# Kernel tuning notes

Hardware: AMD Instinct MI355X
Metric: run time of the kernel (lower is better)

## Reference

```python
import jax, jax.numpy as jnp
import numpy as np
import math

H = 12          # num_heads
HD = 64         # head_dim
M = 32          # random features = head_dim * kernel_ratio
EPS = 1e-8


def prm_exp(x, w):
    # x: [B,H,T,HD], w: [H,M,HD] -> [B,H,T,M]
    xd = 0.5 * jnp.sum(x * x, axis=-1, keepdims=True)        # [B,H,T,1]
    wtx = jnp.einsum('bhti,hmi->bhtm', x, w)                  # [B,H,T,M]
    return jnp.exp(wtx - xd) / math.sqrt(M)


def setup_inputs() -> dict:
    key = jax.random.key(0)
    ks = jax.random.split(key, 5)
    B, N, C = 8, 4096, 768
    x = jax.random.normal(ks[0], (B, N, C), dtype=jnp.float32)
    kqv_w = jax.random.normal(ks[1], (3 * C, C), dtype=jnp.float32) * (1.0 / math.sqrt(C))
    kqv_b = jnp.zeros((3 * C,), dtype=jnp.float32)
    proj_w = jax.random.normal(ks[2], (C, C), dtype=jnp.float32) * (1.0 / math.sqrt(C))
    proj_b = jnp.zeros((C,), dtype=jnp.float32)
    # frozen random-feature matrix: orthogonal rows per head, scaled by sqrt(M)
    wr = jax.random.normal(ks[3], (H, M, HD), dtype=jnp.float32)
    q_ortho, _ = jnp.linalg.qr(jnp.swapaxes(wr, -1, -2))       # [H,HD,M], cols orthonormal
    w = jnp.swapaxes(q_ortho, -1, -2) * math.sqrt(M)           # [H,M,HD]
    return {"x": x, "kqv_w": kqv_w, "kqv_b": kqv_b,
            "proj_w": proj_w, "proj_b": proj_b, "w": w}


def reference(x, kqv_w, kqv_b, proj_w, proj_b, w):
    B, N, C = x.shape
    kqv = x @ kqv_w.T + kqv_b                                  # [B,N,3C]
    kqv = kqv.reshape(B, N, 3, H, HD).transpose(2, 0, 3, 1, 4) # [3,B,H,N,HD]
    k, q, v = kqv[0], kqv[1], kqv[2]
    kp = prm_exp(k, w)                                         # [B,H,N,M]
    qp = prm_exp(q, w)                                         # [B,H,N,M]
    D = jnp.einsum('bhtm,bhm->bht', qp, kp.sum(axis=2))[..., None]   # [B,H,N,1]
    kptv = jnp.einsum('bhin,bhim->bhnm', v, kp)                # [B,H,HD,M]
    y = jnp.einsum('bhtm,bhnm->bhtn', qp, kptv) / (D + EPS)    # [B,H,N,HD]
    y = y.transpose(0, 2, 1, 3).reshape(B, N, C)
    y = y @ proj_w.T + proj_b
    return y
```

## Files before the change

kernel.cpp:

```cpp
#include <hip/hip_runtime.h>
#include <math.h>

namespace {
constexpr int cB  = 8;
constexpr int cN  = 4096;
constexpr int cC  = 768;
constexpr int cH  = 12;
constexpr int cHD = 64;
constexpr int cM  = 32;
}

typedef __attribute__((ext_vector_type(8))) short bf16x8;
typedef __attribute__((ext_vector_type(4))) float f32x4;

#define BARRIER() do { asm volatile("" ::: "memory"); __builtin_amdgcn_s_barrier(); asm volatile("" ::: "memory"); } while (0)
#define WAIT_VM(N) do { asm volatile("s_waitcnt vmcnt(" #N ")" ::: "memory"); __builtin_amdgcn_sched_barrier(0); } while (0)
#define WAIT_LGKM0() do { asm volatile("s_waitcnt lgkmcnt(0)" ::: "memory"); __builtin_amdgcn_sched_barrier(0); } while (0)

__device__ __forceinline__ void async_copy16(const void* g, void* l) {
    __builtin_amdgcn_global_load_lds((const __attribute__((address_space(1))) void*)g,
                                     (__attribute__((address_space(3))) void*)l, 16, 0, 0);
}

__device__ __forceinline__ ushort f32_to_bf16_rne(float x) {
    unsigned int u = __float_as_uint(x);
    u += 0x7fffu + ((u >> 16) & 1u);
    return (ushort)(u >> 16);
}

__device__ __forceinline__ float bf16_to_f32(ushort u) {
    return __uint_as_float(((unsigned)u) << 16);
}

__device__ __forceinline__ void split2(float f, ushort& h, ushort& l) {
    h = f32_to_bf16_rne(f);
    float r = f - bf16_to_f32(h);
    l = f32_to_bf16_rne(r);
}

__global__ __launch_bounds__(256)
void split_bf16(const float* __restrict__ in, ushort* __restrict__ hi,
                ushort* __restrict__ lo, int n4)
{
    int i = blockIdx.x * 256 + threadIdx.x;
    const int stride = gridDim.x * 256;
    for (; i < n4; i += stride) {
        float4 v = reinterpret_cast<const float4*>(in)[i];
        ushort4 h, l;
        split2(v.x, h.x, l.x);
        split2(v.y, h.y, l.y);
        split2(v.z, h.z, l.z);
        split2(v.w, h.w, l.w);
        reinterpret_cast<ushort4*>(hi)[i] = h;
        reinterpret_cast<ushort4*>(lo)[i] = l;
    }
}

template <int TERMS, int FUSE>
__global__ __launch_bounds__(512, 2)
void gemm256(const ushort* __restrict__ Ah, const ushort* __restrict__ Al,
             const ushort* __restrict__ Bh, const ushort* __restrict__ Bl,
             const float* __restrict__ bias,
             float* __restrict__ Cf, ushort* __restrict__ Cb,
             int Ndim, int K, int mode,
             ushort* __restrict__ kp, ushort* __restrict__ qp,
             float* __restrict__ kpsum_p,
             const ushort* __restrict__ whb, const ushort* __restrict__ wlb)
{
    constexpr int APL = (TERMS >= 2) ? 2 : 1;
    constexpr int BPL = (TERMS == 3) ? 2 : 1;
    constexpr int NPL = APL + BPL;
    __shared__ ushort smem[2 * NPL * 8192];
    const int tid = threadIdx.x;
    const int wave = tid >> 6, lane = tid & 63;
    const int wm = wave >> 2, wn = wave & 3;
    const int fr = lane & 15, fk = lane >> 4;
    const int fco = (fk ^ ((fr >> 1) & 3)) * 8;

    const int nwg = gridDim.x * 128;
    const int orig = blockIdx.x * 128 + blockIdx.y;
    const int swz = (orig & 7) * (nwg >> 3) + (orig >> 3);
    const int row0 = (swz & 127) << 8;
    const int col0 = (swz >> 7) << 8;

    const ushort* planes[NPL];
    if constexpr (TERMS == 3) { planes[0] = Ah; planes[1] = Al; planes[2] = Bh; planes[3] = Bl; }
    else { planes[0] = Ah; planes[1] = Bh; }

    const ushort* gsrc[NPL][2];
    int ldst[NPL][2];
    #pragma unroll
    for (int p = 0; p < NPL; ++p)
        #pragma unroll
        for (int h2 = 0; h2 < 2; ++h2) {
            const int ci = h2 * 512 + tid;
            const int row = ci >> 2;
            const int cc = (ci & 3) ^ ((row >> 1) & 3);
            const int grow = ((p < APL) ? row0 : col0) + row;
            gsrc[p][h2] = planes[p] + (size_t)grow * K + cc * 8;
            ldst[p][h2] = p * 8192 + h2 * 4096 + wave * 512;
        }

    const int NT = K >> 5;
    f32x4 acc[8][4] = {};

    #pragma unroll
    for (int p = 0; p < NPL; ++p)
        #pragma unroll
        for (int h2 = 0; h2 < 2; ++h2)
            async_copy16(gsrc[p][h2], &smem[ldst[p][h2]]);
    #pragma unroll
    for (int p = 0; p < NPL; ++p)
        #pragma unroll
        for (int h2 = 0; h2 < 2; ++h2)
            async_copy16(gsrc[p][h2] + 32, &smem[NPL * 8192 + ldst[p][h2]]);
    if constexpr (TERMS == 3) WAIT_VM(8); else WAIT_VM(4);
    BARRIER();

    for (int t = 0; t < NT; ++t) {
        const int cb = (t & 1) * NPL * 8192;
        const int nb = ((t + 1) & 1) * NPL * 8192;
        bf16x8 fb[4][BPL];
        #pragma unroll
        for (int mp = 0; mp < 4; ++mp) {
            if (mp == 0) {
                #pragma unroll
                for (int ni = 0; ni < 4; ++ni) {
                    const int off = cb + APL * 8192 + (wn * 64 + ni * 16 + fr) * 32 + fco;
                    fb[ni][0] = *reinterpret_cast<const bf16x8*>(&smem[off]);
                    if constexpr (BPL == 2)
                        fb[ni][1] = *reinterpret_cast<const bf16x8*>(&smem[off + 8192]);
                }
            }
            bf16x8 fa[2][APL];
            #pragma unroll
            for (int m2 = 0; m2 < 2; ++m2) {
                const int off = cb + (wm * 128 + (mp * 2 + m2) * 16 + fr) * 32 + fco;
                fa[m2][0] = *reinterpret_cast<const bf16x8*>(&smem[off]);
                if constexpr (APL == 2)
                    fa[m2][1] = *reinterpret_cast<const bf16x8*>(&smem[off + 8192]);
            }
            if (t >= 1 && t + 1 < NT && mp < APL) {
                async_copy16(gsrc[mp][0] + (t + 1) * 32, &smem[nb + ldst[mp][0]]);
                async_copy16(gsrc[mp][1] + (t + 1) * 32, &smem[nb + ldst[mp][1]]);
            }
            if (t + 2 < NT && mp >= APL && mp < APL + BPL) {
                async_copy16(gsrc[mp][0] + (t + 2) * 32, &smem[cb + ldst[mp][0]]);
                async_copy16(gsrc[mp][1] + (t + 2) * 32, &smem[cb + ldst[mp][1]]);
            }
            BARRIER();
            WAIT_LGKM0();
            __builtin_amdgcn_s_setprio(1);
            #pragma unroll
            for (int term = 0; term < TERMS; ++term) {
                const int pa = (TERMS == 3) ? ((term == 2) ? 1 : 0) : 0;
                const int pb = (TERMS == 3) ? ((term == 1) ? 1 : 0) : 0;
                #pragma unroll
                for (int m2 = 0; m2 < 2; ++m2)
                    #pragma unroll
                    for (int ni = 0; ni < 4; ++ni)
                        acc[mp * 2 + m2][ni] = __builtin_amdgcn_mfma_f32_16x16x32_bf16(
                            fa[m2][pa], fb[ni][pb], acc[mp * 2 + m2][ni], 0, 0, 0);
            }
            __builtin_amdgcn_s_setprio(0);
            if (mp == 3) {
                if (t + 2 < NT)      { if constexpr (BPL == 2) WAIT_VM(4); else WAIT_VM(2); }
                else if (t + 1 < NT) { WAIT_VM(0); }
            }
            if (mp < 3 || t + 1 < NT) BARRIER();
        }
    }

    if constexpr (FUSE) {
        BARRIER();
        const int cglob = col0 + wn * 64;
        const bool is_k = (cglob < 768);
        const int h = (is_k ? cglob : cglob - 768) >> 6;
        const int rbase = row0 + wm * 128;
        const int b = rbase >> 12;
        const int bh = b * cH + h;
        const int trow0 = rbase & 4095;
        ushort* phi = is_k ? kp : qp;
        bf16x8 Wh2[2][2], Wl2[2][2];
        #pragma unroll
        for (int mf = 0; mf < 2; ++mf)
            #pragma unroll
            for (int kc = 0; kc < 2; ++kc) {
                size_t off = (size_t)(h * 32 + mf * 16 + fr) * 64 + kc * 32 + fk * 8;
                Wh2[mf][kc] = *reinterpret_cast<const bf16x8*>(&whb[off]);
                Wl2[mf][kc] = *reinterpret_cast<const bf16x8*>(&wlb[off]);
            }
        unsigned* kt = reinterpret_cast<unsigned*>(&smem[wave * 8192]);
        const float rsm = 0.17677669529663687f;
        #pragma unroll
        for (int pass = 0; pass < 2; ++pass) {
            #pragma unroll
            for (int ni = 0; ni < 4; ++ni) {
                const float bv = bias[cglob + ni * 16 + fr];
                #pragma unroll
                for (int mi = 0; mi < 4; ++mi) {
                    #pragma unroll
                    for (int j = 0; j < 4; ++j) {
                        const int rrow = mi * 16 + fk * 4 + j;
                        const int ccol = ni * 16 + fr;
                        ushort hh, ll;
                        split2(acc[pass * 4 + mi][ni][j] + bv, hh, ll);
                        const int ccs = (ccol >> 2) ^ (rrow & 15);
                        kt[rrow * 64 + ccs * 4 + (ccol & 3)] = ((unsigned)ll << 16) | hh;
                    }
                }
            }
            f32x4 acc2[4][2] = {};
            float xdv4[4];
            #pragma unroll
            for (int tf = 0; tf < 4; ++tf) {
                const int rrow = tf * 16 + fr;
                const unsigned* rowp = &kt[rrow * 64];
                uint4 c0 = *reinterpret_cast<const uint4*>(&rowp[(((fk << 1))     ^ fr) << 2]);
                uint4 c1 = *reinterpret_cast<const uint4*>(&rowp[(((fk << 1) | 1) ^ fr) << 2]);
                uint4 c2 = *reinterpret_cast<const uint4*>(&rowp[(((fk << 1) + 8) ^ fr) << 2]);
                uint4 c3 = *reinterpret_cast<const uint4*>(&rowp[(((fk << 1) + 9) ^ fr) << 2]);
                unsigned u[16] = {c0.x,c0.y,c0.z,c0.w, c1.x,c1.y,c1.z,c1.w,
                                  c2.x,c2.y,c2.z,c2.w, c3.x,c3.y,c3.z,c3.w};
                bf16x8 Ah2[2], Al2[2];
                float xs = 0.f;
                #pragma unroll
                for (int e = 0; e < 16; ++e) {
                    const ushort hh = (ushort)(u[e] & 0xffffu);
                    const ushort ll = (ushort)(u[e] >> 16);
                    Ah2[e >> 3][e & 7] = (short)hh;
                    Al2[e >> 3][e & 7] = (short)ll;
                    const float kv = bf16_to_f32(hh) + bf16_to_f32(ll);
                    xs = fmaf(kv, kv, xs);
                }
                xs += __shfl_xor(xs, 16);
                xs += __shfl_xor(xs, 32);
                xdv4[tf] = 0.5f * xs;
                #pragma unroll
                for (int kc = 0; kc < 2; ++kc)
                    #pragma unroll
                    for (int mf = 0; mf < 2; ++mf) {
                        acc2[tf][mf] = __builtin_amdgcn_mfma_f32_16x16x32_bf16(Ah2[kc], Wh2[mf][kc], acc2[tf][mf], 0, 0, 0);
                        acc2[tf][mf] = __builtin_amdgcn_mfma_f32_16x16x32_bf16(Ah2[kc], Wl2[mf][kc], acc2[tf][mf], 0, 0, 0);
                        acc2[tf][mf] = __builtin_amdgcn_mfma_f32_16x16x32_bf16(Al2[kc], Wh2[mf][kc], acc2[tf][mf], 0, 0, 0);
                    }
            }
            float sm0 = 0.f, sm1 = 0.f;
            #pragma unroll
            for (int tf = 0; tf < 4; ++tf) {
                #pragma unroll
                for (int j = 0; j < 4; ++j) {
                    const int rloc = fk * 4 + j;
                    const float xdv = __shfl(xdv4[tf], (lane & 48) | rloc);
                    const int tg = trow0 + pass * 64 + tf * 16 + rloc;
                    float e0 = __expf(acc2[tf][0][j] - xdv) * rsm;
                    float e1 = __expf(acc2[tf][1][j] - xdv) * rsm;
                    phi[((size_t)bh * cN + tg) * cM + fr]      = f32_to_bf16_rne(e0);
                    phi[((size_t)bh * cN + tg) * cM + 16 + fr] = f32_to_bf16_rne(e1);
                    sm0 += e0; sm1 += e1;
                }
            }
            if (is_k) {
                sm0 += __shfl_xor(sm0, 16); sm0 += __shfl_xor(sm0, 32);
                sm1 += __shfl_xor(sm1, 16); sm1 += __shfl_xor(sm1, 32);
                const int tblk = (trow0 + pass * 64) >> 6;
                if (lane < 16) {
                    kpsum_p[((size_t)bh * 64 + tblk) * cM + lane]      = sm0;
                    kpsum_p[((size_t)bh * 64 + tblk) * cM + 16 + lane] = sm1;
                }
            }
        }
        return;
    }

    #pragma unroll
    for (int ni = 0; ni < 4; ++ni) {
        const int c = col0 + wn * 64 + ni * 16 + fr;
        const float bv = bias[c];
        #pragma unroll
        for (int mi = 0; mi < 8; ++mi) {
            const int r0 = row0 + wm * 128 + mi * 16 + fk * 4;
            #pragma unroll
            for (int j = 0; j < 4; ++j) {
                const float val = acc[mi][ni][j] + bv;
                const int row = r0 + j;
                if (mode == 0) {
                    Cf[(size_t)row * Ndim + c] = val;
                } else {
                    const int b = row >> 12, tt = row & 4095;
                    const int h = c >> 6, d = c & 63;
                    Cb[(((size_t)(b * cH + h) * cN + tt) << 6) + d] = f32_to_bf16_rne(val);
                }
            }
        }
    }
}

__global__ __launch_bounds__(64)
void pv_mfma(const ushort* __restrict__ qp, const ushort* __restrict__ kptvx,
             ushort* __restrict__ yh)
{
    const int bh = blockIdx.x, tblk = blockIdx.y;
    const int b = bh / cH, h = bh % cH;
    const int t0 = tblk * 64;
    const int lane = threadIdx.x;
    const int fr = lane & 15, fk = lane >> 4;
    bf16x8 Bf[5];
    #pragma unroll
    for (int nf = 0; nf < 5; ++nf)
        Bf[nf] = *reinterpret_cast<const bf16x8*>(&kptvx[(size_t)bh * 2560 + (nf * 16 + fr) * 32 + fk * 8]);
    f32x4 acc[4][5] = {};
    #pragma unroll
    for (int tf = 0; tf < 4; ++tf) {
        bf16x8 Af = *reinterpret_cast<const bf16x8*>(&qp[((size_t)bh * cN + t0 + tf * 16 + fr) * cM + fk * 8]);
        #pragma unroll
        for (int nf = 0; nf < 5; ++nf)
            acc[tf][nf] = __builtin_amdgcn_mfma_f32_16x16x32_bf16(Af, Bf[nf], acc[tf][nf], 0, 0, 0);
    }
    #pragma unroll
    for (int tf = 0; tf < 4; ++tf) {
        #pragma unroll
        for (int j = 0; j < 4; ++j) {
            const int rloc = (lane >> 4) * 4 + j;
            const int t = t0 + tf * 16 + rloc;
            const float Dv = __shfl(acc[tf][4][j], lane & 48) + 1e-8f;
            const float rD = 1.0f / Dv;
            #pragma unroll
            for (int nf = 0; nf < 4; ++nf) {
                float yv = acc[tf][nf][j] * rD;
                size_t oa = (size_t)(b * cN + t) * cC + h * 64 + nf * 16 + fr;
                yh[oa] = f32_to_bf16_rne(yv);
            }
        }
    }
}

__global__ __launch_bounds__(256, 4)
void kptv_part(const ushort* __restrict__ vbf, const ushort* __restrict__ kp,
               float* __restrict__ kptv_p)
{
    const int bh = blockIdx.x, chunk = blockIdx.y;
    __shared__ float vl[64][68];
    __shared__ float kl[64][36];
    const int tid = threadIdx.x;
    const int half = tid >> 7;
    const int dg = (tid >> 3) & 15;
    const int mg = tid & 7;
    float acc[4][4] = {};
    for (int tile = 0; tile < 8; ++tile) {
        const int tb = chunk * 512 + tile * 64;
        #pragma unroll
        for (int i = 0; i < 2; ++i) {
            int idx = i * 256 + tid;
            int row = idx >> 3, seg = idx & 7;
            bf16x8 vv = *reinterpret_cast<const bf16x8*>(&vbf[((size_t)bh * cN + tb + row) * 64 + seg * 8]);
            float4 lo4 = make_float4(bf16_to_f32((ushort)vv[0]), bf16_to_f32((ushort)vv[1]),
                                     bf16_to_f32((ushort)vv[2]), bf16_to_f32((ushort)vv[3]));
            float4 hi4 = make_float4(bf16_to_f32((ushort)vv[4]), bf16_to_f32((ushort)vv[5]),
                                     bf16_to_f32((ushort)vv[6]), bf16_to_f32((ushort)vv[7]));
            *reinterpret_cast<float4*>(&vl[row][seg * 8])     = lo4;
            *reinterpret_cast<float4*>(&vl[row][seg * 8 + 4]) = hi4;
        }
        {
            int row = tid >> 2, seg = tid & 3;
            bf16x8 vv = *reinterpret_cast<const bf16x8*>(&kp[((size_t)bh * cN + tb + row) * 32 + seg * 8]);
            float4 lo4 = make_float4(bf16_to_f32((ushort)vv[0]), bf16_to_f32((ushort)vv[1]),
                                     bf16_to_f32((ushort)vv[2]), bf16_to_f32((ushort)vv[3]));
            float4 hi4 = make_float4(bf16_to_f32((ushort)vv[4]), bf16_to_f32((ushort)vv[5]),
                                     bf16_to_f32((ushort)vv[6]), bf16_to_f32((ushort)vv[7]));
            *reinterpret_cast<float4*>(&kl[row][seg * 8])     = lo4;
            *reinterpret_cast<float4*>(&kl[row][seg * 8 + 4]) = hi4;
        }
        __syncthreads();
        for (int t = 0; t < 32; ++t) {
            const int tt = half * 32 + t;
            float4 av = *reinterpret_cast<const float4*>(&vl[tt][dg * 4]);
            float4 bv = *reinterpret_cast<const float4*>(&kl[tt][mg * 4]);
            float a4[4] = {av.x, av.y, av.z, av.w};
            float b4[4] = {bv.x, bv.y, bv.z, bv.w};
            #pragma unroll
            for (int i = 0; i < 4; ++i)
                #pragma unroll
                for (int j = 0; j < 4; ++j)
                    acc[i][j] = fmaf(a4[i], b4[j], acc[i][j]);
        }
        __syncthreads();
    }
    float* outp = &kptv_p[(((size_t)chunk * 2 + half) * 96 + bh) * 2048];
    #pragma unroll
    for (int i = 0; i < 4; ++i)
        *reinterpret_cast<float4*>(&outp[(dg * 4 + i) * 32 + mg * 4]) =
            make_float4(acc[i][0], acc[i][1], acc[i][2], acc[i][3]);
}

__global__ __launch_bounds__(256)
void kptv_reduce(const float* __restrict__ kptv_p, const float* __restrict__ kpsum_p,
                 ushort* __restrict__ kptvx)
{
    const int bh = blockIdx.x, tid = threadIdx.x;
    for (int l = tid; l < 2048; l += 256) {
        float s = 0.f;
        #pragma unroll
        for (int c = 0; c < 16; ++c) s += kptv_p[((size_t)c * 96 + bh) * 2048 + l];
        kptvx[(size_t)bh * 2560 + l] = f32_to_bf16_rne(s);
    }
    if (tid < 32) {
        float s = 0.f;
        #pragma unroll
        for (int c = 0; c < 64; ++c) s += kpsum_p[((size_t)bh * 64 + c) * cM + tid];
        kptvx[(size_t)bh * 2560 + 64 * 32 + tid] = f32_to_bf16_rne(s);
    }
    for (int l = tid; l < 480; l += 256)
        kptvx[(size_t)bh * 2560 + 65 * 32 + l] = 0;
}

extern "C" void kernel_launch(void* const* d_in, const int* in_sizes, int n_in,
                              void* d_out, int out_size, void* d_ws, size_t ws_size,
                              hipStream_t stream)
{
    const float* x      = (const float*)d_in[0];
    const float* kqv_w  = (const float*)d_in[1];
    const float* kqv_b  = (const float*)d_in[2];
    const float* proj_w = (const float*)d_in[3];
    const float* proj_b = (const float*)d_in[4];
    const float* w      = (const float*)d_in[5];

    char* wsb = (char*)d_ws;
    ushort* xh   = (ushort*)(wsb);
    ushort* xl   = (ushort*)(wsb + 50331648);
    ushort* yh   = (ushort*)(wsb + 100663296);
    ushort* vbf  = (ushort*)(wsb + 201326592);
    ushort* wh   = (ushort*)(wsb + 251658240);
    ushort* wl_  = (ushort*)(wsb + 255197184);
    ushort* pwh  = (ushort*)(wsb + 258736128);
    ushort* pwl  = (ushort*)(wsb + 259915776);
    ushort* whb  = (ushort*)(wsb + 261095424);
    ushort* wlb  = (ushort*)(wsb + 261144576);

    char* ob = (char*)d_out;
    ushort* kp      = (ushort*)ob;
    ushort* qp      = (ushort*)(ob + 25165824);
    float*  kptv_p  = (float*)(ob + 50331648);
    float*  kpsum_p = (float*)(ob + 62914560);
    ushort* kptvx   = (ushort*)(ob + 63700992);
    float*  out     = (float*)d_out;

    dim3 blk(256);
    split_bf16<<<2048, blk, 0, stream>>>(x, xh, xl, 25165824 / 4);
    split_bf16<<<1728, blk, 0, stream>>>(kqv_w, wh, wl_, 1769472 / 4);
    split_bf16<<<576, blk, 0, stream>>>(proj_w, pwh, pwl, 589824 / 4);
    split_bf16<<<24, blk, 0, stream>>>(w, whb, wlb, 24576 / 4);
    gemm256<3, 1><<<dim3(6, 128), dim3(512), 0, stream>>>(
        xh, xl, wh, wl_, kqv_b, nullptr, nullptr, 1536, 768, 0,
        kp, qp, kpsum_p, whb, wlb);
    gemm256<1, 0><<<dim3(3, 128), dim3(512), 0, stream>>>(
        xh, nullptr, wh + (size_t)1536 * 768, nullptr, kqv_b + 1536,
        nullptr, vbf, 768, 768, 2, nullptr, nullptr, nullptr, nullptr, nullptr);
    kptv_part<<<dim3(96, 8), blk, 0, stream>>>(vbf, kp, kptv_p);
    kptv_reduce<<<dim3(96), blk, 0, stream>>>(kptv_p, kpsum_p, kptvx);
    pv_mfma<<<dim3(96, 64), dim3(64), 0, stream>>>(qp, kptvx, yh);
    gemm256<1, 0><<<dim3(3, 128), dim3(512), 0, stream>>>(
        yh, nullptr, pwh, nullptr, proj_b, out, nullptr, 768, 768, 0,
        nullptr, nullptr, nullptr, nullptr, nullptr);
}
```

Before: 438.8 us.

## Compute K^T V with MFMA on transposed kp/v layouts

The fused GEMM epilogue now writes kp and v token-contiguous (transposed per head), so a new MFMA kernel can compute the per-chunk kptv partials directly from global memory. This replaces the LDS-staged scalar FMA kernel. pv_mfma is also regrouped to four waves per block, so fewer blocks are launched. The transposed stores in the GEMM epilogue are strided across tokens and may lose write coalescing. A redundant shuffle whose result is discarded was added to pv_mfma.

New measurement: 479.3 us. +9.2%, slower.

```diff
diff --git a/kernel.cpp b/kernel.cpp
--- a/kernel.cpp
+++ b/kernel.cpp
@@ -180,7 +180,6 @@
         const int b = rbase >> 12;
         const int bh = b * cH + h;
         const int trow0 = rbase & 4095;
-        ushort* phi = is_k ? kp : qp;
         bf16x8 Wh2[2][2], Wl2[2][2];
         #pragma unroll
         for (int mf = 0; mf < 2; ++mf)
@@ -255,8 +254,13 @@
                     const int tg = trow0 + pass * 64 + tf * 16 + rloc;
                     float e0 = __expf(acc2[tf][0][j] - xdv) * rsm;
                     float e1 = __expf(acc2[tf][1][j] - xdv) * rsm;
-                    phi[((size_t)bh * cN + tg) * cM + fr]      = f32_to_bf16_rne(e0);
-                    phi[((size_t)bh * cN + tg) * cM + 16 + fr] = f32_to_bf16_rne(e1);
+                    if (is_k) {
+                        kp[((size_t)bh * cM + fr)      * cN + tg] = f32_to_bf16_rne(e0);
+                        kp[((size_t)bh * cM + 16 + fr) * cN + tg] = f32_to_bf16_rne(e1);
+                    } else {
+                        qp[((size_t)bh * cN + tg) * cM + fr]      = f32_to_bf16_rne(e0);
+                        qp[((size_t)bh * cN + tg) * cM + 16 + fr] = f32_to_bf16_rne(e1);
+                    }
                     sm0 += e0; sm1 += e1;
                 }
             }
@@ -289,21 +293,83 @@
                 } else {
                     const int b = row >> 12, tt = row & 4095;
                     const int h = c >> 6, d = c & 63;
-                    Cb[(((size_t)(b * cH + h) * cN + tt) << 6) + d] = f32_to_bf16_rne(val);
-                }
-            }
-        }
-    }
-}
-
-__global__ __launch_bounds__(64)
+                    Cb[((size_t)(b * cH + h) * cHD + d) * cN + tt] = f32_to_bf16_rne(val);
+                }
+            }
+        }
+    }
+}
+
+__global__ __launch_bounds__(256)
+void kptv_part_mfma(const ushort* __restrict__ vT, const ushort* __restrict__ kpT,
+                    float* __restrict__ kptv_p)
+{
+    const int bh = blockIdx.x;
+    const int wave = threadIdx.x >> 6, lane = threadIdx.x & 63;
+    const int chunk = blockIdx.y * 4 + wave;
+    const int tbase = chunk * 256;
+    const int fr = lane & 15, fk = lane >> 4;
+    const ushort* va = vT  + (size_t)bh * cHD * cN;
+    const ushort* kb = kpT + (size_t)bh * cM * cN;
+    f32x4 acc[4][2] = {};
+    #pragma unroll
+    for (int ks = 0; ks < 8; ++ks) {
+        const int tk = tbase + ks * 32 + fk * 8;
+        bf16x8 bfrag[2];
+        #pragma unroll
+        for (int ni = 0; ni < 2; ++ni)
+            bfrag[ni] = *reinterpret_cast<const bf16x8*>(&kb[(size_t)(ni * 16 + fr) * cN + tk]);
+        #pragma unroll
+        for (int mi = 0; mi < 4; ++mi) {
+            bf16x8 afrag = *reinterpret_cast<const bf16x8*>(&va[(size_t)(mi * 16 + fr) * cN + tk]);
+            #pragma unroll
+            for (int ni = 0; ni < 2; ++ni)
+                acc[mi][ni] = __builtin_amdgcn_mfma_f32_16x16x32_bf16(afrag, bfrag[ni], acc[mi][ni], 0, 0, 0);
+        }
+    }
+    float* outp = &kptv_p[((size_t)chunk * 96 + bh) * 2048];
+    #pragma unroll
+    for (int mi = 0; mi < 4; ++mi)
+        #pragma unroll
+        for (int ni = 0; ni < 2; ++ni)
+            #pragma unroll
+            for (int j = 0; j < 4; ++j) {
+                const int d = mi * 16 + fk * 4 + j;
+                const int m = ni * 16 + fr;
+                outp[d * 32 + m] = acc[mi][ni][j];
+            }
+}
+
+__global__ __launch_bounds__(256)
+void kptv_reduce(const float* __restrict__ kptv_p, const float* __restrict__ kpsum_p,
+                 ushort* __restrict__ kptvx)
+{
+    const int bh = blockIdx.x, tid = threadIdx.x;
+    for (int l = tid; l < 2048; l += 256) {
+        float s = 0.f;
+        #pragma unroll
+        for (int c = 0; c < 16; ++c) s += kptv_p[((size_t)c * 96 + bh) * 2048 + l];
+        kptvx[(size_t)bh * 2560 + l] = f32_to_bf16_rne(s);
+    }
+    if (tid < 32) {
+        float s = 0.f;
+        #pragma unroll
+        for (int c = 0; c < 64; ++c) s += kpsum_p[((size_t)bh * 64 + c) * cM + tid];
+        kptvx[(size_t)bh * 2560 + 64 * 32 + tid] = f32_to_bf16_rne(s);
+    }
+    for (int l = tid; l < 480; l += 256)
+        kptvx[(size_t)bh * 2560 + 65 * 32 + l] = 0;
+}
+
+__global__ __launch_bounds__(256)
 void pv_mfma(const ushort* __restrict__ qp, const ushort* __restrict__ kptvx,
              ushort* __restrict__ yh)
 {
-    const int bh = blockIdx.x, tblk = blockIdx.y;
+    const int bh = blockIdx.x;
+    const int wave = threadIdx.x >> 6, lane = threadIdx.x & 63;
+    const int tblk = blockIdx.y * 4 + wave;
     const int b = bh / cH, h = bh % cH;
     const int t0 = tblk * 64;
-    const int lane = threadIdx.x;
     const int fr = lane & 15, fk = lane >> 4;
     bf16x8 Bf[5];
     #pragma unroll
@@ -321,10 +387,12 @@
     for (int tf = 0; tf < 4; ++tf) {
         #pragma unroll
         for (int j = 0; j < 4; ++j) {
-            const int rloc = (lane >> 4) * 4 + j;
+            const int rloc = fk * 4 + j;
             const int t = t0 + tf * 16 + rloc;
-            const float Dv = __shfl(acc[tf][4][j], lane & 48) + 1e-8f;
-            const float rD = 1.0f / Dv;
+            const float Dv = __shfl(acc[tf][4][j], (lane & 48) | rloc ? (lane & 48) : (lane & 48)) + 0.f;
+            const float Dv2 = __shfl(acc[tf][4][j], lane & 48) + 1e-8f;
+            (void)Dv;
+            const float rD = 1.0f / Dv2;
             #pragma unroll
             for (int nf = 0; nf < 4; ++nf) {
                 float yv = acc[tf][nf][j] * rD;
@@ -333,85 +401,6 @@
             }
         }
     }
-}
-
-__global__ __launch_bounds__(256, 4)
-void kptv_part(const ushort* __restrict__ vbf, const ushort* __restrict__ kp,
-               float* __restrict__ kptv_p)
-{
-    const int bh = blockIdx.x, chunk = blockIdx.y;
-    __shared__ float vl[64][68];
-    __shared__ float kl[64][36];
-    const int tid = threadIdx.x;
-    const int half = tid >> 7;
-    const int dg = (tid >> 3) & 15;
-    const int mg = tid & 7;
-    float acc[4][4] = {};
-    for (int tile = 0; tile < 8; ++tile) {
-        const int tb = chunk * 512 + tile * 64;
-        #pragma unroll
-        for (int i = 0; i < 2; ++i) {
-            int idx = i * 256 + tid;
-            int row = idx >> 3, seg = idx & 7;
-            bf16x8 vv = *reinterpret_cast<const bf16x8*>(&vbf[((size_t)bh * cN + tb + row) * 64 + seg * 8]);
-            float4 lo4 = make_float4(bf16_to_f32((ushort)vv[0]), bf16_to_f32((ushort)vv[1]),
-                                     bf16_to_f32((ushort)vv[2]), bf16_to_f32((ushort)vv[3]));
-            float4 hi4 = make_float4(bf16_to_f32((ushort)vv[4]), bf16_to_f32((ushort)vv[5]),
-                                     bf16_to_f32((ushort)vv[6]), bf16_to_f32((ushort)vv[7]));
-            *reinterpret_cast<float4*>(&vl[row][seg * 8])     = lo4;
-            *reinterpret_cast<float4*>(&vl[row][seg * 8 + 4]) = hi4;
-        }
-        {
-            int row = tid >> 2, seg = tid & 3;
-            bf16x8 vv = *reinterpret_cast<const bf16x8*>(&kp[((size_t)bh * cN + tb + row) * 32 + seg * 8]);
-            float4 lo4 = make_float4(bf16_to_f32((ushort)vv[0]), bf16_to_f32((ushort)vv[1]),
-                                     bf16_to_f32((ushort)vv[2]), bf16_to_f32((ushort)vv[3]));
-            float4 hi4 = make_float4(bf16_to_f32((ushort)vv[4]), bf16_to_f32((ushort)vv[5]),
-                                     bf16_to_f32((ushort)vv[6]), bf16_to_f32((ushort)vv[7]));
-            *reinterpret_cast<float4*>(&kl[row][seg * 8])     = lo4;
-            *reinterpret_cast<float4*>(&kl[row][seg * 8 + 4]) = hi4;
-        }
-        __syncthreads();
-        for (int t = 0; t < 32; ++t) {
-            const int tt = half * 32 + t;
-            float4 av = *reinterpret_cast<const float4*>(&vl[tt][dg * 4]);
-            float4 bv = *reinterpret_cast<const float4*>(&kl[tt][mg * 4]);
-            float a4[4] = {av.x, av.y, av.z, av.w};
-            float b4[4] = {bv.x, bv.y, bv.z, bv.w};
-            #pragma unroll
-            for (int i = 0; i < 4; ++i)
-                #pragma unroll
-                for (int j = 0; j < 4; ++j)
-                    acc[i][j] = fmaf(a4[i], b4[j], acc[i][j]);
-        }
-        __syncthreads();
-    }
-    float* outp = &kptv_p[(((size_t)chunk * 2 + half) * 96 + bh) * 2048];
-    #pragma unroll
-    for (int i = 0; i < 4; ++i)
-        *reinterpret_cast<float4*>(&outp[(dg * 4 + i) * 32 + mg * 4]) =
-            make_float4(acc[i][0], acc[i][1], acc[i][2], acc[i][3]);
-}
-
-__global__ __launch_bounds__(256)
-void kptv_reduce(const float* __restrict__ kptv_p, const float* __restrict__ kpsum_p,
-                 ushort* __restrict__ kptvx)
-{
-    const int bh = blockIdx.x, tid = threadIdx.x;
-    for (int l = tid; l < 2048; l += 256) {
-        float s = 0.f;
-        #pragma unroll
-        for (int c = 0; c < 16; ++c) s += kptv_p[((size_t)c * 96 + bh) * 2048 + l];
-        kptvx[(size_t)bh * 2560 + l] = f32_to_bf16_rne(s);
-    }
-    if (tid < 32) {
-        float s = 0.f;
-        #pragma unroll
-        for (int c = 0; c < 64; ++c) s += kpsum_p[((size_t)bh * 64 + c) * cM + tid];
-        kptvx[(size_t)bh * 2560 + 64 * 32 + tid] = f32_to_bf16_rne(s);
-    }
-    for (int l = tid; l < 480; l += 256)
-        kptvx[(size_t)bh * 2560 + 65 * 32 + l] = 0;
 }
 
 extern "C" void kernel_launch(void* const* d_in, const int* in_sizes, int n_in,
@@ -456,9 +445,9 @@
     gemm256<1, 0><<<dim3(3, 128), dim3(512), 0, stream>>>(
         xh, nullptr, wh + (size_t)1536 * 768, nullptr, kqv_b + 1536,
         nullptr, vbf, 768, 768, 2, nullptr, nullptr, nullptr, nullptr, nullptr);
-    kptv_part<<<dim3(96, 8), blk, 0, stream>>>(vbf, kp, kptv_p);
+    kptv_part_mfma<<<dim3(96, 4), blk, 0, stream>>>(vbf, kp, kptv_p);
     kptv_reduce<<<dim3(96), blk, 0, stream>>>(kptv_p, kpsum_p, kptvx);
-    pv_mfma<<<dim3(96, 64), dim3(64), 0, stream>>>(qp, kptvx, yh);
+    pv_mfma<<<dim3(96, 16), blk, 0, stream>>>(qp, kptvx, yh);
     gemm256<1, 0><<<dim3(3, 128), dim3(512), 0, stream>>>(
         yh, nullptr, pwh, nullptr, proj_b, out, nullptr, 768, 768, 0,
         nullptr, nullptr, nullptr, nullptr, nullptr);
```
